# Performance work log

Hardware: AMD Instinct MI355X
Metric: run time of the kernel (lower is better)

Reference implementation:

```python
import jax, jax.numpy as jnp
import numpy as np

ROPE_THETA = 500000.0


def apply_rope(x, position_ids):
    # x: (B, H, S, hd), position_ids: (B, S)
    hd = x.shape[-1]
    inv_freq = 1.0 / (ROPE_THETA ** (jnp.arange(0, hd, 2, dtype=x.dtype) / hd))  # (hd/2,)
    freqs = position_ids.astype(x.dtype)[:, :, None] * inv_freq  # (B, S, hd/2)
    sin = jnp.sin(freqs)[:, None, :, :]  # (B, 1, S, hd/2)
    cos = jnp.cos(freqs)[:, None, :, :]
    x1 = x[..., ::2]
    x2 = x[..., 1::2]
    even = x1 * cos - x2 * sin
    odd = x2 * cos + x1 * sin
    # interleave even/odd back: stack on a new trailing axis then flatten
    return jnp.stack([even, odd], axis=-1).reshape(x.shape)


def setup_inputs() -> dict:
    key = jax.random.key(0)
    k_x, k_q, k_k, k_v, k_o = jax.random.split(key, 5)
    B, S, D = 2, 2048, 2048
    H, H_kv = 32, 8
    hd = D // H
    x = jax.random.normal(k_x, (B, S, D), dtype=jnp.float32)
    position_ids = jnp.broadcast_to(jnp.arange(S, dtype=jnp.int64)[None, :], (B, S))
    scale = 0.02
    Wq = jax.random.normal(k_q, (D, H * hd), dtype=jnp.float32) * scale
    Wk = jax.random.normal(k_k, (D, H_kv * hd), dtype=jnp.float32) * scale
    Wv = jax.random.normal(k_v, (D, H_kv * hd), dtype=jnp.float32) * scale
    Wo = jax.random.normal(k_o, (D, D), dtype=jnp.float32) * scale
    return {"x": x, "position_ids": position_ids, "Wq": Wq, "Wk": Wk, "Wv": Wv, "Wo": Wo}


def reference(x, position_ids, Wq, Wk, Wv, Wo):
    B, S, D = x.shape
    H, H_kv = 32, 8
    hd = D // H
    G = H // H_kv  # query heads per kv head

    q = (x @ Wq).reshape(B, S, H, hd).transpose(0, 2, 1, 3)        # (B, H, S, hd)
    k = (x @ Wk).reshape(B, S, H_kv, hd).transpose(0, 2, 1, 3)     # (B, H_kv, S, hd)
    v = (x @ Wv).reshape(B, S, H_kv, hd).transpose(0, 2, 1, 3)

    q = apply_rope(q, position_ids)
    k = apply_rope(k, position_ids)

    # GQA: group query heads (B, H_kv, G, S, hd); repeat_interleave maps head h -> kv head h // G
    qg = q.reshape(B, H_kv, G, S, hd)
    scores = jnp.einsum("bkgsh,bkth->bkgst", qg, k) / jnp.sqrt(jnp.asarray(hd, x.dtype))

    causal = jnp.triu(jnp.ones((S, S), dtype=bool), 1)  # True = masked
    scores = jnp.where(causal, jnp.asarray(-jnp.inf, scores.dtype), scores)

    attn = jax.nn.softmax(scores, axis=-1)  # (B, H_kv, G, S, S)
    z = jnp.einsum("bkgst,bkth->bkgsh", attn, v)  # (B, H_kv, G, S, hd)
    z = z.reshape(B, H, S, hd).transpose(0, 2, 1, 3).reshape(B, S, D)
    return z @ Wo
```

## Files before the change

kernel.cpp:

```cpp
#include <hip/hip_runtime.h>
#include <hip/hip_bf16.h>


#define S_LEN 2048
#define DIM   2048
#define NH    32
#define NKV   8
#define HD    64
#define BS    4096
#define NQKV  3072
#define LL(x) ((long long)(x))

typedef __bf16 bf16x8 __attribute__((ext_vector_type(8)));
typedef float  f32x4  __attribute__((ext_vector_type(4)));

__device__ __forceinline__ unsigned short bfb(float f) {
  __hip_bfloat16 h = __float2bfloat16(f);
  return *reinterpret_cast<unsigned short*>(&h);
}

__device__ __forceinline__ unsigned cvtpk(float lo, float hi) {
  unsigned u;
  asm("v_cvt_pk_bf16_f32 %0, %1, %2" : "=v"(u) : "v"(lo), "v"(hi));
  return u;
}

__device__ __forceinline__ void gload16(const void* g, void* l) {
  __builtin_amdgcn_global_load_lds(
      (const __attribute__((address_space(1))) void*)g,
      (__attribute__((address_space(3))) void*)l, 16, 0, 0);
}

__global__ void k_rope_tab(float* __restrict__ tab) {
  int i = blockIdx.x * 256 + threadIdx.x;
  if (i >= S_LEN * 32) return;
  int s = i >> 5, f = i & 31;
  double inv = pow(500000.0, -2.0 * (double)f / 64.0);
  double fr = (double)s * inv;
  tab[2 * i]     = (float)cos(fr);
  tab[2 * i + 1] = (float)sin(fr);
}

__global__ void k_cast4(const float* __restrict__ in, unsigned short* __restrict__ out, int n4) {
  int i = blockIdx.x * 256 + threadIdx.x;
  if (i >= n4) return;
  float4 v = ((const float4*)in)[i];
  ushort4 o;
  o.x = bfb(v.x); o.y = bfb(v.y); o.z = bfb(v.z); o.w = bfb(v.w);
  ((ushort4*)out)[i] = o;
}

__global__ void k_tcast(const float* __restrict__ in, unsigned short* __restrict__ out,
                        int K, int N) {
  __shared__ float tile[32][33];
  int n0 = blockIdx.x * 32, k0 = blockIdx.y * 32;
  int tx = threadIdx.x, ty = threadIdx.y;
#pragma unroll
  for (int r = 0; r < 32; r += 8) tile[ty + r][tx] = in[LL(k0 + ty + r) * N + n0 + tx];
  __syncthreads();
#pragma unroll
  for (int r = 0; r < 32; r += 8) out[LL(n0 + ty + r) * K + k0 + tx] = bfb(tile[tx][ty + r]);
}

__global__ void k_vtrans(const unsigned short* __restrict__ vbuf, unsigned short* __restrict__ vt) {
  __shared__ __align__(16) unsigned short tile[64][72];
  int s0 = blockIdx.x * 64;
  int bh = blockIdx.y;
  int b = bh >> 3, kvh = bh & 7;
  int t = threadIdx.x;
#pragma unroll
  for (int c = t; c < 512; c += 256) {
    int s = c >> 3, seg = c & 7;
    *(uint4*)&tile[s][seg * 8] =
        *(const uint4*)(vbuf + LL(b * S_LEN + s0 + s) * (NKV * HD) + kvh * HD + seg * 8);
  }
  __syncthreads();
#pragma unroll
  for (int c = t; c < 512; c += 256) {
    int d = c >> 3, sseg = c & 7;
    ushort4 x0, x1;
    unsigned short* xp = (unsigned short*)&x0;
#pragma unroll
    for (int j = 0; j < 4; j++) xp[j] = tile[sseg * 8 + j][d];
    unsigned short* yp = (unsigned short*)&x1;
#pragma unroll
    for (int j = 0; j < 4; j++) yp[j] = tile[sseg * 8 + 4 + j][d];
    uint4 o;
    o.x = ((unsigned*)&x0)[0]; o.y = ((unsigned*)&x0)[1];
    o.z = ((unsigned*)&x1)[0]; o.w = ((unsigned*)&x1)[1];
    *(uint4*)(vt + (LL(bh) * HD + d) * S_LEN + s0 + sseg * 8) = o;
  }
}

template <int MODE>
__global__ __launch_bounds__(256, 2) void k_gemm(
    const unsigned short* __restrict__ A, const unsigned short* __restrict__ Bt,
    void* __restrict__ Cout, int M, int N, int K,
    const float* __restrict__ tab, unsigned short* __restrict__ qbuf,
    unsigned short* __restrict__ kbuf, unsigned short* __restrict__ vbuf) {
  __shared__ __align__(16) unsigned short As[128 * 32];
  __shared__ __align__(16) unsigned short Bs[128 * 32];
  int t = threadIdx.x;
  int lane = t & 63, w = t >> 6;
  int wr = w >> 1, wc = w & 1;
  int g = lane >> 4, r = lane & 15;
  int gx = gridDim.x;
  int nwg = gx * gridDim.y;
  int lin = blockIdx.y * gx + blockIdx.x;
  int cpx = nwg >> 3;
  int swz = (lin & 7) * cpx + (lin >> 3);
  int bx = swz % gx, by = swz / gx;
  long long rowBase = LL(by) * 128;
  long long colBase = LL(bx) * 128;

  f32x4 acc[4][4] = {};

  int c0 = t, c1 = t + 256;
  const unsigned short* ag0 = A + (rowBase + (c0 >> 2)) * K + (c0 & 3) * 8;
  const unsigned short* ag1 = A + (rowBase + (c1 >> 2)) * K + (c1 & 3) * 8;
  const unsigned short* bg0 = Bt + (colBase + (c0 >> 2)) * K + (c0 & 3) * 8;
  const unsigned short* bg1 = Bt + (colBase + (c1 >> 2)) * K + (c1 & 3) * 8;
  char* lA0 = (char*)As + c0 * 16; char* lA1 = (char*)As + c1 * 16;
  char* lB0 = (char*)Bs + c0 * 16; char* lB1 = (char*)Bs + c1 * 16;

  for (int kt = 0; kt < K; kt += 32) {
    __syncthreads();
    gload16(ag0 + kt, lA0);
    gload16(ag1 + kt, lA1);
    gload16(bg0 + kt, lB0);
    gload16(bg1 + kt, lB1);
    __syncthreads();

    bf16x8 af[4], bfr[4];
#pragma unroll
    for (int m = 0; m < 4; m++)
      af[m] = *(const bf16x8*)(const void*)(As + (wr * 64 + m * 16 + r) * 32 + g * 8);
#pragma unroll
    for (int n = 0; n < 4; n++)
      bfr[n] = *(const bf16x8*)(const void*)(Bs + (wc * 64 + n * 16 + r) * 32 + g * 8);
#pragma unroll
    for (int m = 0; m < 4; m++)
#pragma unroll
      for (int n = 0; n < 4; n++)
        acc[m][n] = __builtin_amdgcn_mfma_f32_16x16x32_bf16(af[m], bfr[n], acc[m][n], 0, 0, 0);
  }

  if (MODE == 0) {
#pragma unroll
    for (int m = 0; m < 4; m++)
#pragma unroll
      for (int n = 0; n < 4; n++) {
        long long row0 = rowBase + wr * 64 + m * 16 + g * 4;
        long long col = colBase + wc * 64 + n * 16 + r;
#pragma unroll
        for (int j = 0; j < 4; j++)
          ((float*)Cout)[(row0 + j) * N + col] = acc[m][n][j];
      }
  } else {
#pragma unroll
    for (int n = 0; n < 4; n++) {
      int gc0 = (int)colBase + wc * 64 + n * 16;
      int gc = gc0 + r;
      unsigned short* dst; int dcol, dstride; float scale; bool rope;
      if (gc0 < 2048)      { dst = qbuf; dcol = gc;        dstride = DIM; scale = 0.18033688f; rope = true; }
      else if (gc0 < 2560) { dst = kbuf; dcol = gc - 2048; dstride = 512; scale = 1.0f;        rope = true; }
      else                 { dst = vbuf; dcol = gc - 2560; dstride = 512; scale = 1.0f;        rope = false; }
      int f = (gc & 63) >> 1;
      float sgn = (gc & 1) ? 1.f : -1.f;
#pragma unroll
      for (int m = 0; m < 4; m++) {
        long long row0 = rowBase + wr * 64 + m * 16 + g * 4;
#pragma unroll
        for (int j = 0; j < 4; j++) {
          float v = acc[m][n][j];
          float o;
          if (rope) {
            float part = __shfl_xor(v, 1);
            int s = (int)((row0 + j) & (S_LEN - 1));
            float cc = tab[(s * 32 + f) * 2], ss = tab[(s * 32 + f) * 2 + 1];
            o = (v * cc + sgn * part * ss) * scale;
          } else o = v;
          dst[(row0 + j) * dstride + dcol] = bfb(o);
        }
      }
    }
  }
}

__global__ __launch_bounds__(256, 4) void k_attn(
    const unsigned short* __restrict__ qb, const unsigned short* __restrict__ kb,
    const unsigned short* __restrict__ vt, unsigned short* __restrict__ zb) {
  int pair = blockIdx.x;
  int h = blockIdx.y, b = blockIdx.z;
  int kvh = h >> 2, bh = b * NKV + kvh;
  int t = threadIdx.x, lane = t & 63, w = t >> 6;
  int g = lane >> 4, r = lane & 15;
  int sw = (r & 7) * 8;

  __shared__ __align__(16) unsigned short Ks[2][64 * 64];
  __shared__ __align__(16) unsigned short Vs[2][64 * 64];
  __shared__ __align__(16) unsigned short Ps[4][16 * 64];

  unsigned short* Pw = Ps[w];

  int c0 = t, c1 = t + 256;
  const unsigned short* kg0 = kb + LL(b) * S_LEN * 512 + (c0 >> 3) * 512 + kvh * HD
                                 + (((c0 & 7) ^ ((c0 >> 3) & 7)) * 8);
  const unsigned short* kg1 = kb + LL(b) * S_LEN * 512 + (c1 >> 3) * 512 + kvh * HD
                                 + (((c1 & 7) ^ ((c1 >> 3) & 7)) * 8);
  const unsigned short* vg0 = vt + (LL(bh) * HD + (c0 >> 3)) * S_LEN
                                 + (((c0 & 7) ^ ((c0 >> 3) & 7)) * 8);
  const unsigned short* vg1 = vt + (LL(bh) * HD + (c1 >> 3)) * S_LEN
                                 + (((c1 & 7) ^ ((c1 >> 3) & 7)) * 8);

#define STAGE(bufi, kst_)                                              \
  {                                                                    \
    gload16(kg0 + LL(kst_) * 512, (char*)Ks[bufi] + c0 * 16);          \
    gload16(kg1 + LL(kst_) * 512, (char*)Ks[bufi] + c1 * 16);          \
    gload16(vg0 + (kst_), (char*)Vs[bufi] + c0 * 16);                  \
    gload16(vg1 + (kst_), (char*)Vs[bufi] + c1 * 16);                  \
  }

#pragma unroll 1
  for (int pass = 0; pass < 2; pass++) {
    int qt = pass ? (31 - pair) : pair;
    int qbase = qt * 64;
    int qglob = qbase + w * 16 + r;
    long long qrow = LL(b) * S_LEN + qglob;

    bf16x8 qf[2];
    qf[0] = *(const bf16x8*)(const void*)(qb + qrow * DIM + h * HD + g * 8);
    qf[1] = *(const bf16x8*)(const void*)(qb + qrow * DIM + h * HD + 32 + g * 8);

    f32x4 acc[4] = {};
    float mrun = -1e30f, lrun = 0.f;

    int nt = qt + 1;
    __syncthreads();
    STAGE(0, 0);
    for (int tt = 0; tt < nt; tt++) {
      int kst = tt * 64;
      int cur = tt & 1;
      if (tt + 1 < nt) {
        STAGE(cur ^ 1, kst + 64);
        asm volatile("s_waitcnt vmcnt(4)" ::: "memory");
      } else {
        asm volatile("s_waitcnt vmcnt(0)" ::: "memory");
      }
      __builtin_amdgcn_s_barrier();
      __builtin_amdgcn_sched_barrier(0);

      const unsigned short* Kc = Ks[cur];
      const unsigned short* Vc = Vs[cur];

      bf16x8 kfr[4][2];
#pragma unroll
      for (int nf = 0; nf < 4; nf++)
#pragma unroll
        for (int kd = 0; kd < 2; kd++)
          kfr[nf][kd] = *(const bf16x8*)(const void*)(
              Kc + (nf * 16 + r) * 64 + ((kd * 32 + g * 8) ^ sw));

      __builtin_amdgcn_s_setprio(1);
      f32x4 sc[4] = {};
#pragma unroll
      for (int nf = 0; nf < 4; nf++)
#pragma unroll
        for (int kd = 0; kd < 2; kd++)
          sc[nf] = __builtin_amdgcn_mfma_f32_16x16x32_bf16(
              kfr[nf][kd], qf[kd], sc[nf], 0, 0, 0);
      __builtin_amdgcn_s_setprio(0);

      bf16x8 vfr[4][2];
#pragma unroll
      for (int d = 0; d < 4; d++)
#pragma unroll
        for (int ks = 0; ks < 2; ks++)
          vfr[d][ks] = *(const bf16x8*)(const void*)(
              Vc + (d * 16 + r) * 64 + ((ks * 32 + g * 8) ^ sw));

      if (tt == nt - 1) {
#pragma unroll
        for (int nf = 0; nf < 4; nf++)
#pragma unroll
          for (int j = 0; j < 4; j++)
            if (kst + nf * 16 + g * 4 + j > qglob) sc[nf][j] = -1e30f;
      }

      float pm = fmaxf(fmaxf(fmaxf(sc[0][0], sc[0][1]), fmaxf(sc[0][2], sc[0][3])),
                       fmaxf(fmaxf(sc[1][0], sc[1][1]), fmaxf(sc[1][2], sc[1][3])));
      pm = fmaxf(pm, fmaxf(fmaxf(fmaxf(sc[2][0], sc[2][1]), fmaxf(sc[2][2], sc[2][3])),
                           fmaxf(fmaxf(sc[3][0], sc[3][1]), fmaxf(sc[3][2], sc[3][3]))));
      pm = fmaxf(pm, __shfl_xor(pm, 16));
      pm = fmaxf(pm, __shfl_xor(pm, 32));
      if (__any(pm > mrun + 12.0f)) {
        float mnew = fmaxf(mrun, pm);
        float al = exp2f(mrun - mnew);
        mrun = mnew;
        lrun *= al;
#pragma unroll
        for (int d = 0; d < 4; d++) acc[d] *= al;
      }
      float ls = 0.f;
#pragma unroll
      for (int nf = 0; nf < 4; nf++) {
        float p0 = exp2f(sc[nf][0] - mrun);
        float p1 = exp2f(sc[nf][1] - mrun);
        float p2 = exp2f(sc[nf][2] - mrun);
        float p3 = exp2f(sc[nf][3] - mrun);
        ls += (p0 + p1) + (p2 + p3);
        uint2 u;
        u.x = cvtpk(p0, p1);
        u.y = cvtpk(p2, p3);
        *(uint2*)(void*)(Pw + r * 64 + ((nf * 16 + g * 4) ^ sw)) = u;
      }
      ls += __shfl_xor(ls, 16);
      ls += __shfl_xor(ls, 32);
      lrun += ls;

      bf16x8 pf[2];
      pf[0] = *(const bf16x8*)(const void*)(Pw + r * 64 + ((g * 8) ^ sw));
      pf[1] = *(const bf16x8*)(const void*)(Pw + r * 64 + ((32 + g * 8) ^ sw));
      __builtin_amdgcn_s_setprio(1);
#pragma unroll
      for (int d = 0; d < 4; d++)
#pragma unroll
        for (int ks = 0; ks < 2; ks++)
          acc[d] = __builtin_amdgcn_mfma_f32_16x16x32_bf16(
              vfr[d][ks], pf[ks], acc[d], 0, 0, 0);
      __builtin_amdgcn_s_setprio(0);

      __builtin_amdgcn_sched_barrier(0);
      __builtin_amdgcn_s_barrier();
    }

    float inv = 1.0f / lrun;
#pragma unroll
    for (int d = 0; d < 4; d++) {
      uint2 u;
      u.x = cvtpk(acc[d][0] * inv, acc[d][1] * inv);
      u.y = cvtpk(acc[d][2] * inv, acc[d][3] * inv);
      *(uint2*)(void*)(zb + qrow * DIM + h * HD + d * 16 + g * 4) = u;
    }
  }
#undef STAGE
}

extern "C" void kernel_launch(void* const* d_in, const int* in_sizes, int n_in,
                              void* d_out, int out_size, void* d_ws, size_t ws_size,
                              hipStream_t stream) {
  const float* x  = (const float*)d_in[0];
  const float* Wq = (const float*)d_in[2];
  const float* Wk = (const float*)d_in[3];
  const float* Wv = (const float*)d_in[4];
  const float* Wo = (const float*)d_in[5];
  float* out = (float*)d_out;

  char* wsb = (char*)d_ws;
  size_t off = 0;
  auto alloc = [&](size_t bytes) {
    void* p = wsb + off;
    off += (bytes + 255) & ~(size_t)255;
    return p;
  };
  float* tab            = (float*)alloc(LL(S_LEN) * 32 * 2 * 4);
  unsigned short* xb    = (unsigned short*)alloc(LL(BS) * DIM * 2);
  unsigned short* wqkvt = (unsigned short*)alloc(LL(NQKV) * DIM * 2);
  unsigned short* wot   = (unsigned short*)alloc(LL(DIM) * DIM * 2);
  unsigned short* qbuf  = (unsigned short*)alloc(LL(BS) * DIM * 2);
  unsigned short* kbuf  = (unsigned short*)alloc(LL(BS) * (NKV * HD) * 2);
  unsigned short* vbuf  = (unsigned short*)alloc(LL(BS) * (NKV * HD) * 2);
  unsigned short* vtb   = (unsigned short*)alloc(LL(2 * NKV) * HD * S_LEN * 2);
  unsigned short* zb    = (unsigned short*)alloc(LL(BS) * DIM * 2);

  k_rope_tab<<<(S_LEN * 32 + 255) / 256, 256, 0, stream>>>(tab);
  k_cast4<<<(BS * DIM / 4 + 255) / 256, 256, 0, stream>>>(x, xb, BS * DIM / 4);
  k_tcast<<<dim3(DIM / 32, DIM / 32), dim3(32, 8), 0, stream>>>(Wq, wqkvt, DIM, DIM);
  k_tcast<<<dim3(512 / 32, DIM / 32), dim3(32, 8), 0, stream>>>(Wk, wqkvt + LL(2048) * DIM, DIM, 512);
  k_tcast<<<dim3(512 / 32, DIM / 32), dim3(32, 8), 0, stream>>>(Wv, wqkvt + LL(2560) * DIM, DIM, 512);
  k_tcast<<<dim3(DIM / 32, DIM / 32), dim3(32, 8), 0, stream>>>(Wo, wot, DIM, DIM);

  k_gemm<2><<<dim3(NQKV / 128, BS / 128), 256, 0, stream>>>(
      xb, wqkvt, nullptr, BS, NQKV, DIM, tab, qbuf, kbuf, vbuf);

  k_vtrans<<<dim3(S_LEN / 64, 2 * NKV), 256, 0, stream>>>(vbuf, vtb);

  k_attn<<<dim3(16, NH, 2), 256, 0, stream>>>(qbuf, kbuf, vtb, zb);

  k_gemm<0><<<dim3(DIM / 128, BS / 128), 256, 0, stream>>>(
      zb, wot, out, BS, DIM, DIM, nullptr, nullptr, nullptr, nullptr);
}
```

Measured before the change: 230.0 us.

## Enlarge attention query tile to 128 rows, two 16-row chunks per wave

The attention kernel now processes a 128-row query tile per block, with each wave handling two 16-row chunks that share the K/V fragments loaded from LDS per 64-key tile. This halves global K/V staging traffic per query row and the number of barriers per unit of work. The price is more registers (launch bounds lowered to 2 blocks per CU), fewer blocks in the grid, and some wasted waves on diagonal tiles, which are skipped via a causal check.

```diff
diff --git a/kernel.cpp b/kernel.cpp
--- a/kernel.cpp
+++ b/kernel.cpp
@@ -187,7 +187,7 @@
   }
 }
 
-__global__ __launch_bounds__(256, 4) void k_attn(
+__global__ __launch_bounds__(256, 2) void k_attn(
     const unsigned short* __restrict__ qb, const unsigned short* __restrict__ kb,
     const unsigned short* __restrict__ vt, unsigned short* __restrict__ zb) {
   int pair = blockIdx.x;
@@ -199,9 +199,7 @@
 
   __shared__ __align__(16) unsigned short Ks[2][64 * 64];
   __shared__ __align__(16) unsigned short Vs[2][64 * 64];
-  __shared__ __align__(16) unsigned short Ps[4][16 * 64];
-
-  unsigned short* Pw = Ps[w];
+  __shared__ __align__(16) unsigned short Ps[4][2][16 * 64];
 
   int c0 = t, c1 = t + 256;
   const unsigned short* kg0 = kb + LL(b) * S_LEN * 512 + (c0 >> 3) * 512 + kvh * HD
@@ -223,19 +221,23 @@
 
 #pragma unroll 1
   for (int pass = 0; pass < 2; pass++) {
-    int qt = pass ? (31 - pair) : pair;
-    int qbase = qt * 64;
-    int qglob = qbase + w * 16 + r;
-    long long qrow = LL(b) * S_LEN + qglob;
-
-    bf16x8 qf[2];
-    qf[0] = *(const bf16x8*)(const void*)(qb + qrow * DIM + h * HD + g * 8);
-    qf[1] = *(const bf16x8*)(const void*)(qb + qrow * DIM + h * HD + 32 + g * 8);
-
-    f32x4 acc[4] = {};
-    float mrun = -1e30f, lrun = 0.f;
-
-    int nt = qt + 1;
+    int st = pass ? (15 - pair) : pair;
+    int qbase = st * 128;
+    int rowb = qbase + w * 32;
+
+    bf16x8 qf[2][2];
+#pragma unroll
+    for (int c = 0; c < 2; c++) {
+      long long qr = LL(b) * S_LEN + rowb + c * 16 + r;
+      qf[c][0] = *(const bf16x8*)(const void*)(qb + qr * DIM + h * HD + g * 8);
+      qf[c][1] = *(const bf16x8*)(const void*)(qb + qr * DIM + h * HD + 32 + g * 8);
+    }
+
+    f32x4 acc[2][4] = {};
+    float mrun[2] = {-1e30f, -1e30f};
+    float lrun[2] = {0.f, 0.f};
+
+    int nt = 2 * st + 2;
     __syncthreads();
     STAGE(0, 0);
     for (int tt = 0; tt < nt; tt++) {
@@ -250,97 +252,107 @@
       __builtin_amdgcn_s_barrier();
       __builtin_amdgcn_sched_barrier(0);
 
-      const unsigned short* Kc = Ks[cur];
-      const unsigned short* Vc = Vs[cur];
-
-      bf16x8 kfr[4][2];
-#pragma unroll
-      for (int nf = 0; nf < 4; nf++)
-#pragma unroll
-        for (int kd = 0; kd < 2; kd++)
-          kfr[nf][kd] = *(const bf16x8*)(const void*)(
-              Kc + (nf * 16 + r) * 64 + ((kd * 32 + g * 8) ^ sw));
-
-      __builtin_amdgcn_s_setprio(1);
-      f32x4 sc[4] = {};
-#pragma unroll
-      for (int nf = 0; nf < 4; nf++)
-#pragma unroll
-        for (int kd = 0; kd < 2; kd++)
-          sc[nf] = __builtin_amdgcn_mfma_f32_16x16x32_bf16(
-              kfr[nf][kd], qf[kd], sc[nf], 0, 0, 0);
-      __builtin_amdgcn_s_setprio(0);
-
-      bf16x8 vfr[4][2];
-#pragma unroll
-      for (int d = 0; d < 4; d++)
-#pragma unroll
-        for (int ks = 0; ks < 2; ks++)
-          vfr[d][ks] = *(const bf16x8*)(const void*)(
-              Vc + (d * 16 + r) * 64 + ((ks * 32 + g * 8) ^ sw));
-
-      if (tt == nt - 1) {
+      if (kst <= rowb + 31) {
+        const unsigned short* Kc = Ks[cur];
+        const unsigned short* Vc = Vs[cur];
+
+        bf16x8 kfr[4][2], vfr[4][2];
 #pragma unroll
         for (int nf = 0; nf < 4; nf++)
 #pragma unroll
-          for (int j = 0; j < 4; j++)
-            if (kst + nf * 16 + g * 4 + j > qglob) sc[nf][j] = -1e30f;
+          for (int kd = 0; kd < 2; kd++)
+            kfr[nf][kd] = *(const bf16x8*)(const void*)(
+                Kc + (nf * 16 + r) * 64 + ((kd * 32 + g * 8) ^ sw));
+#pragma unroll
+        for (int d = 0; d < 4; d++)
+#pragma unroll
+          for (int ks = 0; ks < 2; ks++)
+            vfr[d][ks] = *(const bf16x8*)(const void*)(
+                Vc + (d * 16 + r) * 64 + ((ks * 32 + g * 8) ^ sw));
+
+#pragma unroll
+        for (int c = 0; c < 2; c++) {
+          unsigned short* Pw = Ps[w][c];
+          int qg = rowb + c * 16 + r;
+
+          __builtin_amdgcn_s_setprio(1);
+          f32x4 sc[4] = {};
+#pragma unroll
+          for (int nf = 0; nf < 4; nf++)
+#pragma unroll
+            for (int kd = 0; kd < 2; kd++)
+              sc[nf] = __builtin_amdgcn_mfma_f32_16x16x32_bf16(
+                  kfr[nf][kd], qf[c][kd], sc[nf], 0, 0, 0);
+          __builtin_amdgcn_s_setprio(0);
+
+          if (kst + 63 > rowb + c * 16) {
+#pragma unroll
+            for (int nf = 0; nf < 4; nf++)
+#pragma unroll
+              for (int j = 0; j < 4; j++)
+                if (kst + nf * 16 + g * 4 + j > qg) sc[nf][j] = -1e30f;
+          }
+
+          float pm = fmaxf(fmaxf(fmaxf(sc[0][0], sc[0][1]), fmaxf(sc[0][2], sc[0][3])),
+                           fmaxf(fmaxf(sc[1][0], sc[1][1]), fmaxf(sc[1][2], sc[1][3])));
+          pm = fmaxf(pm, fmaxf(fmaxf(fmaxf(sc[2][0], sc[2][1]), fmaxf(sc[2][2], sc[2][3])),
+                               fmaxf(fmaxf(sc[3][0], sc[3][1]), fmaxf(sc[3][2], sc[3][3]))));
+          pm = fmaxf(pm, __shfl_xor(pm, 16));
+          pm = fmaxf(pm, __shfl_xor(pm, 32));
+          if (__any(pm > mrun[c] + 12.0f)) {
+            float mnew = fmaxf(mrun[c], pm);
+            float al = exp2f(mrun[c] - mnew);
+            mrun[c] = mnew;
+            lrun[c] *= al;
+#pragma unroll
+            for (int d = 0; d < 4; d++) acc[c][d] *= al;
+          }
+          float ls = 0.f;
+#pragma unroll
+          for (int nf = 0; nf < 4; nf++) {
+            float p0 = exp2f(sc[nf][0] - mrun[c]);
+            float p1 = exp2f(sc[nf][1] - mrun[c]);
+            float p2 = exp2f(sc[nf][2] - mrun[c]);
+            float p3 = exp2f(sc[nf][3] - mrun[c]);
+            ls += (p0 + p1) + (p2 + p3);
+            uint2 u;
+            u.x = cvtpk(p0, p1);
+            u.y = cvtpk(p2, p3);
+            *(uint2*)(void*)(Pw + r * 64 + ((nf * 16 + g * 4) ^ sw)) = u;
+          }
+          ls += __shfl_xor(ls, 16);
+          ls += __shfl_xor(ls, 32);
+          lrun[c] += ls;
+
+          bf16x8 pf[2];
+          pf[0] = *(const bf16x8*)(const void*)(Pw + r * 64 + ((g * 8) ^ sw));
+          pf[1] = *(const bf16x8*)(const void*)(Pw + r * 64 + ((32 + g * 8) ^ sw));
+          __builtin_amdgcn_s_setprio(1);
+#pragma unroll
+          for (int d = 0; d < 4; d++)
+#pragma unroll
+            for (int ks = 0; ks < 2; ks++)
+              acc[c][d] = __builtin_amdgcn_mfma_f32_16x16x32_bf16(
+                  vfr[d][ks], pf[ks], acc[c][d], 0, 0, 0);
+          __builtin_amdgcn_s_setprio(0);
+        }
       }
-
-      float pm = fmaxf(fmaxf(fmaxf(sc[0][0], sc[0][1]), fmaxf(sc[0][2], sc[0][3])),
-                       fmaxf(fmaxf(sc[1][0], sc[1][1]), fmaxf(sc[1][2], sc[1][3])));
-      pm = fmaxf(pm, fmaxf(fmaxf(fmaxf(sc[2][0], sc[2][1]), fmaxf(sc[2][2], sc[2][3])),
-                           fmaxf(fmaxf(sc[3][0], sc[3][1]), fmaxf(sc[3][2], sc[3][3]))));
-      pm = fmaxf(pm, __shfl_xor(pm, 16));
-      pm = fmaxf(pm, __shfl_xor(pm, 32));
-      if (__any(pm > mrun + 12.0f)) {
-        float mnew = fmaxf(mrun, pm);
-        float al = exp2f(mrun - mnew);
-        mrun = mnew;
-        lrun *= al;
-#pragma unroll
-        for (int d = 0; d < 4; d++) acc[d] *= al;
-      }
-      float ls = 0.f;
-#pragma unroll
-      for (int nf = 0; nf < 4; nf++) {
-        float p0 = exp2f(sc[nf][0] - mrun);
-        float p1 = exp2f(sc[nf][1] - mrun);
-        float p2 = exp2f(sc[nf][2] - mrun);
-        float p3 = exp2f(sc[nf][3] - mrun);
-        ls += (p0 + p1) + (p2 + p3);
-        uint2 u;
-        u.x = cvtpk(p0, p1);
-        u.y = cvtpk(p2, p3);
-        *(uint2*)(void*)(Pw + r * 64 + ((nf * 16 + g * 4) ^ sw)) = u;
-      }
-      ls += __shfl_xor(ls, 16);
-      ls += __shfl_xor(ls, 32);
-      lrun += ls;
-
-      bf16x8 pf[2];
-      pf[0] = *(const bf16x8*)(const void*)(Pw + r * 64 + ((g * 8) ^ sw));
-      pf[1] = *(const bf16x8*)(const void*)(Pw + r * 64 + ((32 + g * 8) ^ sw));
-      __builtin_amdgcn_s_setprio(1);
-#pragma unroll
-      for (int d = 0; d < 4; d++)
-#pragma unroll
-        for (int ks = 0; ks < 2; ks++)
-          acc[d] = __builtin_amdgcn_mfma_f32_16x16x32_bf16(
-              vfr[d][ks], pf[ks], acc[d], 0, 0, 0);
-      __builtin_amdgcn_s_setprio(0);
 
       __builtin_amdgcn_sched_barrier(0);
       __builtin_amdgcn_s_barrier();
     }
 
-    float inv = 1.0f / lrun;
-#pragma unroll
-    for (int d = 0; d < 4; d++) {
-      uint2 u;
-      u.x = cvtpk(acc[d][0] * inv, acc[d][1] * inv);
-      u.y = cvtpk(acc[d][2] * inv, acc[d][3] * inv);
-      *(uint2*)(void*)(zb + qrow * DIM + h * HD + d * 16 + g * 4) = u;
+#pragma unroll
+    for (int c = 0; c < 2; c++) {
+      float inv = 1.0f / lrun[c];
+      long long qr = LL(b) * S_LEN + rowb + c * 16 + r;
+#pragma unroll
+      for (int d = 0; d < 4; d++) {
+        uint2 u;
+        u.x = cvtpk(acc[c][d][0] * inv, acc[c][d][1] * inv);
+        u.y = cvtpk(acc[c][d][2] * inv, acc[c][d][3] * inv);
+        *(uint2*)(void*)(zb + qr * DIM + h * HD + d * 16 + g * 4) = u;
+      }
     }
   }
 #undef STAGE
@@ -385,7 +397,7 @@
 
   k_vtrans<<<dim3(S_LEN / 64, 2 * NKV), 256, 0, stream>>>(vbuf, vtb);
 
-  k_attn<<<dim3(16, NH, 2), 256, 0, stream>>>(qbuf, kbuf, vtb, zb);
+  k_attn<<<dim3(8, NH, 2), 256, 0, stream>>>(qbuf, kbuf, vtb, zb);
 
   k_gemm<0><<<dim3(DIM / 128, BS / 128), 256, 0, stream>>>(
       zb, wot, out, BS, DIM, DIM, nullptr, nullptr, nullptr, nullptr);
```

Measured after the change: 239.7 us. +4.2%, slower.
